# Performance work log

Hardware: AMD Instinct MI355X
Metric: run time of the kernel (lower is better)

## Reference

```python
import jax, jax.numpy as jnp
import numpy as np

BS, N, F_IN, H, F_OUT = 4, 2048, 128, 4, 64


def setup_inputs() -> dict:
    key = jax.random.key(0)
    k1, k2, k3, k4, k5 = jax.random.split(key, 5)
    x = jax.random.normal(k1, (BS, N, F_IN), dtype=jnp.float32)
    adj = jax.random.randint(k2, (BS, N, N), 0, 2).astype(bool)
    # guarantee self-loops so no softmax row is all -inf
    adj = jnp.logical_or(adj, jnp.eye(N, dtype=bool)[None])
    # xavier-uniform-ish scales
    w = jax.random.uniform(k3, (H, F_IN, F_OUT), dtype=jnp.float32,
                           minval=-1.0, maxval=1.0) * np.sqrt(6.0 / (F_IN + F_OUT))
    a_src = jax.random.uniform(k4, (H, F_OUT, 1), dtype=jnp.float32,
                               minval=-1.0, maxval=1.0) * np.sqrt(6.0 / (F_OUT + 1))
    a_dst = jax.random.uniform(k5, (H, F_OUT, 1), dtype=jnp.float32,
                               minval=-1.0, maxval=1.0) * np.sqrt(6.0 / (F_OUT + 1))
    bias = jnp.zeros((F_OUT,), dtype=jnp.float32)
    return {"x": x, "adj": adj, "w": w, "a_src": a_src, "a_dst": a_dst, "bias": bias}


def reference(x, adj, w, a_src, a_dst, bias):
    bs, n = x.shape[:2]
    # h_prime: [bs, H, n, F_OUT]
    h = jnp.einsum('bnf,hfo->bhno', x, w)
    th = jnp.tanh(h)
    s_src = jnp.einsum('bhno,ho->bhn', th, a_src[..., 0])  # [bs,H,n]
    s_dst = jnp.einsum('bhno,ho->bhn', th, a_dst[..., 0])  # [bs,H,n]
    # attn[b,h,i,j] = src[b,h,i] + dst[b,h,j]
    attn = s_src[..., :, None] + s_dst[..., None, :]
    attn = jnp.where(attn >= 0, attn, 0.2 * attn)  # leaky_relu(0.2)
    attn = jnp.where(adj[:, None], attn, -jnp.inf)  # mask = ~adj
    p = jax.nn.softmax(attn, axis=-1)  # dropout is identity at eval
    out = jnp.einsum('bhij,bhjo->bhio', p, h) + bias  # [bs,H,n,F_OUT]
    # torch .view(bs, n, -1) on contiguous [bs,H,n,F_OUT]: raw reshape
    return out.reshape(bs, n, -1)
```

## Files before the change

kernel.cpp:

```cpp
#include <hip/hip_runtime.h>
#include <hip/hip_fp16.h>

#define NN   2048
#define FIN  128
#define FOUT 64
#define LOG2E 1.44269504088896f

using f16x8 = __attribute__((ext_vector_type(8))) _Float16;
using f16x4 = __attribute__((ext_vector_type(4))) _Float16;
using f16x2 = __attribute__((ext_vector_type(2))) _Float16;
using f32x4 = __attribute__((ext_vector_type(4))) float;
using i32x4 = __attribute__((ext_vector_type(4))) int;

__device__ inline float fast_exp2(float x) {
#if __has_builtin(__builtin_amdgcn_exp2f)
    return __builtin_amdgcn_exp2f(x);
#else
    return exp2f(x);
#endif
}


__global__ __launch_bounds__(256) void k1_proj(
    const float* __restrict__ x, const float* __restrict__ w,
    const float* __restrict__ a_src, const float* __restrict__ a_dst,
    const int* __restrict__ adj,
    _Float16* __restrict__ h16B, float* __restrict__ ssrc, float* __restrict__ sdst,
    unsigned int* __restrict__ adjbits)
{
    __shared__ __align__(16) float w_s[FIN * FOUT];
    __shared__ __align__(16) float xs[64 * 132];

    const int t    = threadIdx.x;
    const int bx   = blockIdx.x;
    const int bh   = bx >> 5;
    const int tile = bx & 31;
    const int b    = bh >> 2;
    const int h    = bh & 3;
    const int n0   = tile * 64;

    {
        const f32x4* wg = (const f32x4*)(w + h * FIN * FOUT);
        f32x4* wl = (f32x4*)w_s;
#pragma unroll
        for (int k = 0; k < 8; ++k) wl[t + 256 * k] = wg[t + 256 * k];
    }
    {
#pragma unroll
        for (int k = 0; k < 8; ++k) {
            int q  = t + 256 * k;
            int r  = q >> 5;
            int c4 = q & 31;
            f32x4 v = *(const f32x4*)(x + (size_t)(b * NN + n0 + r) * FIN + c4 * 4);
            *(f32x4*)(xs + r * 132 + c4 * 4) = v;
        }
    }
    __syncthreads();

    const int ty = t >> 4, tx = t & 15;
    float acc[4][4] = {};

#pragma unroll 4
    for (int f4 = 0; f4 < 32; ++f4) {
        f32x4 xv[4], wv[4];
#pragma unroll
        for (int q = 0; q < 4; ++q)
            xv[q] = *(const f32x4*)(xs + (ty * 4 + q) * 132 + f4 * 4);
#pragma unroll
        for (int k = 0; k < 4; ++k)
            wv[k] = *(const f32x4*)(w_s + (f4 * 4 + k) * 64 + tx * 4);
#pragma unroll
        for (int q = 0; q < 4; ++q)
#pragma unroll
            for (int k = 0; k < 4; ++k)
#pragma unroll
                for (int c = 0; c < 4; ++c)
                    acc[q][c] += xv[q][k] * wv[k][c];
    }

    const int j0 = n0 + ty * 4;
#pragma unroll
    for (int cc = 0; cc < 4; ++cc) {
        int o = tx * 4 + cc;
        f16x4 hv;
#pragma unroll
        for (int q = 0; q < 4; ++q) hv[q] = (_Float16)acc[q][cc];
        int off = bh * 131072 + (j0 >> 5) * 2048 + (o >> 4) * 512
                + (((j0 >> 3) & 3) * 16 + (o & 15)) * 8 + (j0 & 7);
        *(f16x4*)(h16B + off) = hv;
    }

    f32x4 a_s = *(const f32x4*)(a_src + h * FOUT + tx * 4);
    f32x4 a_d = *(const f32x4*)(a_dst + h * FOUT + tx * 4);
    float ss[4], sd[4];
#pragma unroll
    for (int q = 0; q < 4; ++q) {
        float s1 = 0.f, s2 = 0.f;
#pragma unroll
        for (int cc = 0; cc < 4; ++cc) {
            float th = tanhf(acc[q][cc]);
            s1 += th * a_s[cc];
            s2 += th * a_d[cc];
        }
        ss[q] = s1; sd[q] = s2;
    }
#pragma unroll
    for (int m = 1; m <= 8; m <<= 1) {
#pragma unroll
        for (int q = 0; q < 4; ++q) {
            ss[q] += __shfl_xor(ss[q], m);
            sd[q] += __shfl_xor(sd[q], m);
        }
    }
    if (tx == 0) {
#pragma unroll
        for (int q = 0; q < 4; ++q) {
            ssrc[bh * NN + j0 + q] = ss[q] * LOG2E;
            sdst[bh * NN + j0 + q] = sd[q] * LOG2E;
        }
    }

    {
        const int  frow0 = bx * 16;
        const int* asrc  = adj + (size_t)frow0 * NN;
#pragma unroll
        for (int w4 = 0; w4 < 4; ++w4) {
            int widx  = t + 256 * w4;
            int row_l = widx >> 6;
            int wc    = widx & 63;
            const i32x4* p = (const i32x4*)(asrc + (size_t)row_l * NN + wc * 32);
            unsigned int wbits = 0;
#pragma unroll
            for (int k = 0; k < 8; ++k) {
                i32x4 v = p[k];
                wbits |= (unsigned int)(v[0] & 1) << (4 * k);
                wbits |= (unsigned int)(v[1] & 1) << (4 * k + 1);
                wbits |= (unsigned int)(v[2] & 1) << (4 * k + 2);
                wbits |= (unsigned int)(v[3] & 1) << (4 * k + 3);
            }
            adjbits[(size_t)(frow0 + row_l) * 64 + wc] = wbits;
        }
    }
}

__global__ __launch_bounds__(512, 6) void k2_attn(
    const unsigned int* __restrict__ adjbits,
    const _Float16* __restrict__ h16B,
    const float* __restrict__ ssrc, const float* __restrict__ sdst,
    const float* __restrict__ bias, float* __restrict__ out)
{
    __shared__ __align__(16) char smem[50240];
    _Float16*     Bf     = (_Float16*)smem;
    unsigned int* adjw   = (unsigned int*)(smem + 16384);
    float*        E1f    = (float*)(smem + 33792);
    float*        E2f    = (float*)(smem + 41984);
    float*        redmax = (float*)(smem + 50176);
    float*        comb   = (float*)smem;

    const int t    = threadIdx.x;
    const int wv   = t >> 6;
    const int lane = t & 63;
    const int bh   = blockIdx.x >> 5;
    const int i0   = (blockIdx.x & 31) << 6;
    const int b    = bh >> 2;
    const int rg   = wv >> 1;
    const int par  = wv & 1;
    const int m    = lane & 15;
    const int g    = lane >> 4;

    const _Float16* Bsrc = h16B + bh * 131072;

#define STAGE(bufi_, s_)                                                        \
    __builtin_amdgcn_global_load_lds(                                           \
        (const __attribute__((address_space(1))) unsigned int*)(Bsrc + (s_) * 4096 + t * 8), \
        (__attribute__((address_space(3))) unsigned int*)(Bf + (bufi_) * 4096 + t * 8), \
        16, 0, 0)

    STAGE(0, 0);

    {
        const uint4* asrc = (const uint4*)(adjbits + ((size_t)b * NN + i0) * 64);
#pragma unroll
        for (int k = 0; k < 2; ++k) {
            int idx = t + 512 * k;
            uint4 v = asrc[idx];
            unsigned int* dst = adjw + (idx >> 4) * 68 + (idx & 15) * 4;
            *(uint4*)dst = v;
        }
    }
    float dm;
    {
        f32x4 dv = *(const f32x4*)(sdst + bh * NN + t * 4);
        f32x4 e1v, e2v;
#pragma unroll
        for (int e = 0; e < 4; ++e) {
            e1v[e] = fast_exp2(dv[e]);
            e2v[e] = fast_exp2(0.2f * dv[e]);
        }
        *(f32x4*)(E1f + t * 4) = e1v;
        *(f32x4*)(E2f + t * 4) = e2v;
        dm = fmaxf(fmaxf(dv[0], dv[1]), fmaxf(dv[2], dv[3]));
#pragma unroll
        for (int msk = 1; msk <= 32; msk <<= 1) dm = fmaxf(dm, __shfl_xor(dm, msk));
        if (lane == 0) redmax[wv] = dm;
    }
    asm volatile("s_waitcnt vmcnt(0)" ::: "memory");
    __syncthreads();

    float D = redmax[0];
#pragma unroll
    for (int k = 1; k < 8; ++k) D = fmaxf(D, redmax[k]);

    const int row = i0 + rg * 16 + m;
    const float sA = ssrc[bh * NN + row];
    float c = sA + D; c = fmaxf(c, 0.2f * c);
    const float K1 = fast_exp2(sA - c);
    const float K2 = fast_exp2(fmaf(0.2f, sA, -c));

    f32x4 acc0 = {0,0,0,0}, acc1 = {0,0,0,0}, acc2 = {0,0,0,0}, acc3 = {0,0,0,0};
    f32x4 accz = {0,0,0,0};
    f16x8 ones;
#pragma unroll
    for (int i = 0; i < 8; ++i) ones[i] = (_Float16)1.0f;

    const int arow68 = (rg * 16 + m) * 68;

    for (int s = 0; s < 32; ++s) {
        if (s < 31) {
            STAGE((s + 1) & 1, s + 1);
            asm volatile("s_waitcnt vmcnt(1)" ::: "memory");
        } else {
            asm volatile("s_waitcnt vmcnt(0)" ::: "memory");
        }
        __builtin_amdgcn_sched_barrier(0);
        __builtin_amdgcn_s_barrier();
        __builtin_amdgcn_sched_barrier(0);

        const int ci = 2 * s + par;
        unsigned int wb = adjw[arow68 + ci] >> (8 * g);
        const float* e1p = E1f + ci * 32 + 8 * g;
        const float* e2p = E2f + ci * 32 + 8 * g;
        f32x4 e1a = *(const f32x4*)(e1p);
        f32x4 e1b = *(const f32x4*)(e1p + 4);
        f32x4 e2a = *(const f32x4*)(e2p);
        f32x4 e2b = *(const f32x4*)(e2p + 4);

        const _Float16* bb = Bf + (s & 1) * 4096 + par * 2048 + lane * 8;
        f16x8 b0 = *(const f16x8*)(bb);
        f16x8 b1 = *(const f16x8*)(bb + 512);
        f16x8 b2 = *(const f16x8*)(bb + 1024);
        f16x8 b3 = *(const f16x8*)(bb + 1536);

        float ev[8];
#pragma unroll
        for (int i = 0; i < 8; ++i) {
            float E1v = (i < 4) ? e1a[i] : e1b[i - 4];
            float E2v = (i < 4) ? e2a[i] : e2b[i - 4];
            float ee  = fmaxf(K1 * E1v, K2 * E2v);
            ev[i] = (wb & (1u << i)) ? ee : 0.0f;
        }
        union { f16x8 v; f16x2 p[4]; } af;
#pragma unroll
        for (int i = 0; i < 4; ++i)
            af.p[i] = __builtin_bit_cast(f16x2,
                __builtin_amdgcn_cvt_pkrtz(ev[2 * i], ev[2 * i + 1]));

        acc0 = __builtin_amdgcn_mfma_f32_16x16x32_f16(af.v, b0, acc0, 0, 0, 0);
        acc1 = __builtin_amdgcn_mfma_f32_16x16x32_f16(af.v, b1, acc1, 0, 0, 0);
        acc2 = __builtin_amdgcn_mfma_f32_16x16x32_f16(af.v, b2, acc2, 0, 0, 0);
        acc3 = __builtin_amdgcn_mfma_f32_16x16x32_f16(af.v, b3, acc3, 0, 0, 0);
        accz = __builtin_amdgcn_mfma_f32_16x16x32_f16(af.v, ones, accz, 0, 0, 0);

        __builtin_amdgcn_s_barrier();
    }
#undef STAGE

    __syncthreads();
    if (par == 1) {
        float* cp = comb + (rg * 64 + lane) * 20;
#pragma unroll
        for (int r = 0; r < 4; ++r) {
            cp[0 + r]  = acc0[r];
            cp[4 + r]  = acc1[r];
            cp[8 + r]  = acc2[r];
            cp[12 + r] = acc3[r];
            cp[16 + r] = accz[r];
        }
    }
    __syncthreads();
    if (par == 0) {
        const float* cp = comb + (rg * 64 + lane) * 20;
        float zs[4];
#pragma unroll
        for (int r = 0; r < 4; ++r) zs[r] = accz[r] + cp[16 + r];
        size_t obase = ((size_t)bh * NN + i0 + rg * 16) * FOUT;
#pragma unroll
        for (int ot = 0; ot < 4; ++ot) {
            float bv = bias[ot * 16 + m];
            f32x4 a = (ot == 0) ? acc0 : (ot == 1) ? acc1 : (ot == 2) ? acc2 : acc3;
#pragma unroll
            for (int r = 0; r < 4; ++r) {
                float v = (a[r] + cp[ot * 4 + r]) / zs[r] + bv;
                out[obase + (size_t)(g * 4 + r) * FOUT + ot * 16 + m] = v;
            }
        }
    }
}

extern "C" void kernel_launch(void* const* d_in, const int* in_sizes, int n_in,
                              void* d_out, int out_size, void* d_ws, size_t ws_size,
                              hipStream_t stream) {
    (void)in_sizes; (void)n_in; (void)out_size; (void)ws_size;
    const float* x     = (const float*)d_in[0];
    const int*   adj   = (const int*)d_in[1];
    const float* w     = (const float*)d_in[2];
    const float* a_src = (const float*)d_in[3];
    const float* a_dst = (const float*)d_in[4];
    const float* bias  = (const float*)d_in[5];
    float*       out   = (float*)d_out;

    _Float16*     h16B    = (_Float16*)d_ws;
    float*        ssrc    = (float*)((char*)d_ws + 4194304);
    float*        sdst    = (float*)((char*)d_ws + 4194304 + 131072);
    unsigned int* adjbits = (unsigned int*)((char*)d_ws + 4718592);

    k1_proj<<<512, 256, 0, stream>>>(x, w, a_src, a_dst, adj, h16B, ssrc, sdst, adjbits);
    k2_attn<<<512, 512, 0, stream>>>(adjbits, h16B, ssrc, sdst, bias, out);
}
```

Measured before the change: 50.58 us.

## Use MFMA fp16 projection, fast tanh, and packed fp16 attention weights

The projection kernel now converts x and w to fp16 in shared memory and computes the projection with MFMA instructions instead of scalar fp32 FMAs, and replaces tanhf with an exp2/rcp approximation. The attention kernel stores the exp tables in fp16, computes the attention weights with packed fp16 multiply/max plus a bitmask in place of per-element fp32 selects, and fully unrolls the main loop. This is meant to cut ALU and LDS work in both kernels. In exchange it loses precision in the projection, the scores, and the weight products (K times E is now computed in fp16, which could underflow or overflow), and the unroll grows code size.

```diff
diff --git a/kernel.cpp b/kernel.cpp
--- a/kernel.cpp
+++ b/kernel.cpp
@@ -18,6 +18,33 @@
 #else
     return exp2f(x);
 #endif
+}
+__device__ inline float fast_rcp(float x) {
+#if __has_builtin(__builtin_amdgcn_rcpf)
+    return __builtin_amdgcn_rcpf(x);
+#else
+    return 1.0f / x;
+#endif
+}
+__device__ inline float fast_tanh(float x) {
+    float e = fast_exp2(2.0f * LOG2E * x);
+    return 1.0f - 2.0f * fast_rcp(e + 1.0f);
+}
+__device__ inline unsigned cvt2h(float a, float b) {
+    return __builtin_bit_cast(unsigned, __builtin_amdgcn_cvt_pkrtz(a, b));
+}
+__device__ inline f16x2 pkmax(f16x2 a, f16x2 b) {
+#if __has_builtin(__builtin_elementwise_max)
+    return __builtin_elementwise_max(a, b);
+#else
+    f16x2 r; r[0] = a[0] > b[0] ? a[0] : b[0]; r[1] = a[1] > b[1] ? a[1] : b[1];
+    return r;
+#endif
+}
+__device__ inline unsigned bmask(unsigned wb, int p) {
+    unsigned lo = (unsigned)(-(int)((wb >> (2 * p)) & 1u));
+    unsigned hi = (unsigned)(-(int)((wb >> (2 * p + 1)) & 1u));
+    return (hi & 0xFFFF0000u) | (lo & 0x0000FFFFu);
 }
 
 
@@ -28,8 +55,8 @@
     _Float16* __restrict__ h16B, float* __restrict__ ssrc, float* __restrict__ sdst,
     unsigned int* __restrict__ adjbits)
 {
-    __shared__ __align__(16) float w_s[FIN * FOUT];
-    __shared__ __align__(16) float xs[64 * 132];
+    __shared__ __align__(16) _Float16 xf[8192];
+    __shared__ __align__(16) _Float16 wf[8192];
 
     const int t    = threadIdx.x;
     const int bx   = blockIdx.x;
@@ -38,85 +65,88 @@
     const int b    = bh >> 2;
     const int h    = bh & 3;
     const int n0   = tile * 64;
-
-    {
-        const f32x4* wg = (const f32x4*)(w + h * FIN * FOUT);
-        f32x4* wl = (f32x4*)w_s;
-#pragma unroll
-        for (int k = 0; k < 8; ++k) wl[t + 256 * k] = wg[t + 256 * k];
-    }
-    {
-#pragma unroll
-        for (int k = 0; k < 8; ++k) {
-            int q  = t + 256 * k;
-            int r  = q >> 5;
-            int c4 = q & 31;
-            f32x4 v = *(const f32x4*)(x + (size_t)(b * NN + n0 + r) * FIN + c4 * 4);
-            *(f32x4*)(xs + r * 132 + c4 * 4) = v;
+    const int wv   = t >> 6;
+    const int lane = t & 63;
+    const int m    = lane & 15;
+    const int g    = lane >> 4;
+
+    {
+        const int o  = t & 63;
+        const int kc = t >> 6;
+        const float* wcol = w + h * FIN * FOUT + o;
+        _Float16* dst = wf + ((kc * 4 + (o >> 4)) * 512) + (o & 15) * 8;
+#pragma unroll
+        for (int hi = 0; hi < 4; ++hi) {
+            unsigned u0 = cvt2h(wcol[(kc * 32 + hi * 8 + 0) * FOUT],
+                                wcol[(kc * 32 + hi * 8 + 1) * FOUT]);
+            unsigned u1 = cvt2h(wcol[(kc * 32 + hi * 8 + 2) * FOUT],
+                                wcol[(kc * 32 + hi * 8 + 3) * FOUT]);
+            unsigned u2 = cvt2h(wcol[(kc * 32 + hi * 8 + 4) * FOUT],
+                                wcol[(kc * 32 + hi * 8 + 5) * FOUT]);
+            unsigned u3 = cvt2h(wcol[(kc * 32 + hi * 8 + 6) * FOUT],
+                                wcol[(kc * 32 + hi * 8 + 7) * FOUT]);
+            *(uint4*)(dst + hi * 128) = uint4{u0, u1, u2, u3};
+        }
+    }
+    {
+        const int r  = t >> 2;
+        const int kc = t & 3;
+        const float* xr = x + ((size_t)(b * NN + n0 + r)) * FIN + kc * 32;
+        _Float16* dst = xf + ((r >> 4) * 16 + kc * 4) * 128 + (r & 15) * 8;
+#pragma unroll
+        for (int g2 = 0; g2 < 4; ++g2) {
+            f32x4 va = *(const f32x4*)(xr + g2 * 8);
+            f32x4 vb = *(const f32x4*)(xr + g2 * 8 + 4);
+            *(uint4*)(dst + g2 * 128) = uint4{cvt2h(va[0], va[1]), cvt2h(va[2], va[3]),
+                                              cvt2h(vb[0], vb[1]), cvt2h(vb[2], vb[3])};
         }
     }
     __syncthreads();
 
-    const int ty = t >> 4, tx = t & 15;
-    float acc[4][4] = {};
-
-#pragma unroll 4
-    for (int f4 = 0; f4 < 32; ++f4) {
-        f32x4 xv[4], wv[4];
-#pragma unroll
-        for (int q = 0; q < 4; ++q)
-            xv[q] = *(const f32x4*)(xs + (ty * 4 + q) * 132 + f4 * 4);
-#pragma unroll
-        for (int k = 0; k < 4; ++k)
-            wv[k] = *(const f32x4*)(w_s + (f4 * 4 + k) * 64 + tx * 4);
-#pragma unroll
-        for (int q = 0; q < 4; ++q)
-#pragma unroll
-            for (int k = 0; k < 4; ++k)
-#pragma unroll
-                for (int c = 0; c < 4; ++c)
-                    acc[q][c] += xv[q][k] * wv[k][c];
-    }
-
-    const int j0 = n0 + ty * 4;
-#pragma unroll
-    for (int cc = 0; cc < 4; ++cc) {
-        int o = tx * 4 + cc;
-        f16x4 hv;
-#pragma unroll
-        for (int q = 0; q < 4; ++q) hv[q] = (_Float16)acc[q][cc];
-        int off = bh * 131072 + (j0 >> 5) * 2048 + (o >> 4) * 512
-                + (((j0 >> 3) & 3) * 16 + (o & 15)) * 8 + (j0 & 7);
-        *(f16x4*)(h16B + off) = hv;
-    }
-
-    f32x4 a_s = *(const f32x4*)(a_src + h * FOUT + tx * 4);
-    f32x4 a_d = *(const f32x4*)(a_dst + h * FOUT + tx * 4);
-    float ss[4], sd[4];
-#pragma unroll
-    for (int q = 0; q < 4; ++q) {
-        float s1 = 0.f, s2 = 0.f;
-#pragma unroll
-        for (int cc = 0; cc < 4; ++cc) {
-            float th = tanhf(acc[q][cc]);
-            s1 += th * a_s[cc];
-            s2 += th * a_d[cc];
-        }
-        ss[q] = s1; sd[q] = s2;
-    }
-#pragma unroll
-    for (int m = 1; m <= 8; m <<= 1) {
-#pragma unroll
-        for (int q = 0; q < 4; ++q) {
-            ss[q] += __shfl_xor(ss[q], m);
-            sd[q] += __shfl_xor(sd[q], m);
-        }
-    }
-    if (tx == 0) {
-#pragma unroll
-        for (int q = 0; q < 4; ++q) {
-            ssrc[bh * NN + j0 + q] = ss[q] * LOG2E;
-            sdst[bh * NN + j0 + q] = sd[q] * LOG2E;
+    const int rg = wv;
+    f32x4 acc0 = {0,0,0,0}, acc1 = {0,0,0,0}, acc2 = {0,0,0,0}, acc3 = {0,0,0,0};
+#pragma unroll
+    for (int kc = 0; kc < 4; ++kc) {
+        f16x8 av = *(const f16x8*)(xf + (rg * 16 + kc * 4 + g) * 128 + m * 8);
+        const _Float16* wb_ = wf + kc * 4 * 512 + lane * 8;
+        acc0 = __builtin_amdgcn_mfma_f32_16x16x32_f16(av, *(const f16x8*)(wb_), acc0, 0, 0, 0);
+        acc1 = __builtin_amdgcn_mfma_f32_16x16x32_f16(av, *(const f16x8*)(wb_ + 512), acc1, 0, 0, 0);
+        acc2 = __builtin_amdgcn_mfma_f32_16x16x32_f16(av, *(const f16x8*)(wb_ + 1024), acc2, 0, 0, 0);
+        acc3 = __builtin_amdgcn_mfma_f32_16x16x32_f16(av, *(const f16x8*)(wb_ + 1536), acc3, 0, 0, 0);
+    }
+
+    float s1r[4] = {0,0,0,0}, s2r[4] = {0,0,0,0};
+    const int jg = n0 + rg * 16 + g * 4;
+#define PROC(accX, ot)  do {                                                    \
+        float asv = a_src[h * FOUT + (ot) * 16 + m];                            \
+        float adv = a_dst[h * FOUT + (ot) * 16 + m];                            \
+        _Pragma("unroll")                                                       \
+        for (int r = 0; r < 4; ++r) {                                           \
+            float th = fast_tanh(accX[r]);                                      \
+            s1r[r] += th * asv;                                                 \
+            s2r[r] += th * adv;                                                 \
+        }                                                                       \
+        unsigned u0 = cvt2h(accX[0], accX[1]);                                  \
+        unsigned u1 = cvt2h(accX[2], accX[3]);                                  \
+        int off = bh * 131072 + (jg >> 5) * 2048 + (ot) * 512                   \
+                + (((jg >> 3) & 3) * 16 + m) * 8 + (jg & 7);                    \
+        *(uint2*)(h16B + off) = uint2{u0, u1};                                  \
+    } while (0)
+    PROC(acc0, 0); PROC(acc1, 1); PROC(acc2, 2); PROC(acc3, 3);
+#undef PROC
+#pragma unroll
+    for (int msk = 1; msk <= 8; msk <<= 1) {
+#pragma unroll
+        for (int r = 0; r < 4; ++r) {
+            s1r[r] += __shfl_xor(s1r[r], msk);
+            s2r[r] += __shfl_xor(s2r[r], msk);
+        }
+    }
+    if (m == 0) {
+#pragma unroll
+        for (int r = 0; r < 4; ++r) {
+            ssrc[bh * NN + jg + r] = s1r[r] * LOG2E;
+            sdst[bh * NN + jg + r] = s2r[r] * LOG2E;
         }
     }
 
@@ -149,12 +179,12 @@
     const float* __restrict__ ssrc, const float* __restrict__ sdst,
     const float* __restrict__ bias, float* __restrict__ out)
 {
-    __shared__ __align__(16) char smem[50240];
+    __shared__ __align__(16) char smem[42016];
     _Float16*     Bf     = (_Float16*)smem;
     unsigned int* adjw   = (unsigned int*)(smem + 16384);
-    float*        E1f    = (float*)(smem + 33792);
-    float*        E2f    = (float*)(smem + 41984);
-    float*        redmax = (float*)(smem + 50176);
+    _Float16*     E1h    = (_Float16*)(smem + 33792);
+    _Float16*     E2h    = (_Float16*)(smem + 37888);
+    float*        redmax = (float*)(smem + 41984);
     float*        comb   = (float*)smem;
 
     const int t    = threadIdx.x;
@@ -177,28 +207,22 @@
         16, 0, 0)
 
     STAGE(0, 0);
-
     {
         const uint4* asrc = (const uint4*)(adjbits + ((size_t)b * NN + i0) * 64);
 #pragma unroll
         for (int k = 0; k < 2; ++k) {
             int idx = t + 512 * k;
             uint4 v = asrc[idx];
-            unsigned int* dst = adjw + (idx >> 4) * 68 + (idx & 15) * 4;
-            *(uint4*)dst = v;
+            *(uint4*)(adjw + (idx >> 4) * 68 + (idx & 15) * 4) = v;
         }
     }
     float dm;
     {
         f32x4 dv = *(const f32x4*)(sdst + bh * NN + t * 4);
-        f32x4 e1v, e2v;
-#pragma unroll
-        for (int e = 0; e < 4; ++e) {
-            e1v[e] = fast_exp2(dv[e]);
-            e2v[e] = fast_exp2(0.2f * dv[e]);
-        }
-        *(f32x4*)(E1f + t * 4) = e1v;
-        *(f32x4*)(E2f + t * 4) = e2v;
+        *(uint2*)(E1h + t * 4) = uint2{cvt2h(fast_exp2(dv[0]), fast_exp2(dv[1])),
+                                       cvt2h(fast_exp2(dv[2]), fast_exp2(dv[3]))};
+        *(uint2*)(E2h + t * 4) = uint2{cvt2h(fast_exp2(0.2f * dv[0]), fast_exp2(0.2f * dv[1])),
+                                       cvt2h(fast_exp2(0.2f * dv[2]), fast_exp2(0.2f * dv[3]))};
         dm = fmaxf(fmaxf(dv[0], dv[1]), fmaxf(dv[2], dv[3]));
 #pragma unroll
         for (int msk = 1; msk <= 32; msk <<= 1) dm = fmaxf(dm, __shfl_xor(dm, msk));
@@ -214,8 +238,10 @@
     const int row = i0 + rg * 16 + m;
     const float sA = ssrc[bh * NN + row];
     float c = sA + D; c = fmaxf(c, 0.2f * c);
-    const float K1 = fast_exp2(sA - c);
-    const float K2 = fast_exp2(fmaf(0.2f, sA, -c));
+    const float K1f = fast_exp2(sA - c);
+    const float K2f = fast_exp2(fmaf(0.2f, sA, -c));
+    f16x2 K1h2; { _Float16 q = (_Float16)K1f; K1h2[0] = q; K1h2[1] = q; }
+    f16x2 K2h2; { _Float16 q = (_Float16)K2f; K2h2[0] = q; K2h2[1] = q; }
 
     f32x4 acc0 = {0,0,0,0}, acc1 = {0,0,0,0}, acc2 = {0,0,0,0}, acc3 = {0,0,0,0};
     f32x4 accz = {0,0,0,0};
@@ -225,6 +251,7 @@
 
     const int arow68 = (rg * 16 + m) * 68;
 
+#pragma unroll
     for (int s = 0; s < 32; ++s) {
         if (s < 31) {
             STAGE((s + 1) & 1, s + 1);
@@ -237,13 +264,10 @@
         __builtin_amdgcn_sched_barrier(0);
 
         const int ci = 2 * s + par;
-        unsigned int wb = adjw[arow68 + ci] >> (8 * g);
-        const float* e1p = E1f + ci * 32 + 8 * g;
-        const float* e2p = E2f + ci * 32 + 8 * g;
-        f32x4 e1a = *(const f32x4*)(e1p);
-        f32x4 e1b = *(const f32x4*)(e1p + 4);
-        f32x4 e2a = *(const f32x4*)(e2p);
-        f32x4 e2b = *(const f32x4*)(e2p + 4);
+        unsigned wb = adjw[arow68 + ci] >> (8 * g);
+        union { f16x8 v; f16x2 p[4]; unsigned u[4]; } E1u, E2u, af;
+        E1u.v = *(const f16x8*)(E1h + ci * 32 + 8 * g);
+        E2u.v = *(const f16x8*)(E2h + ci * 32 + 8 * g);
 
         const _Float16* bb = Bf + (s & 1) * 4096 + par * 2048 + lane * 8;
         f16x8 b0 = *(const f16x8*)(bb);
@@ -251,19 +275,13 @@
         f16x8 b2 = *(const f16x8*)(bb + 1024);
         f16x8 b3 = *(const f16x8*)(bb + 1536);
 
-        float ev[8];
-#pragma unroll
-        for (int i = 0; i < 8; ++i) {
-            float E1v = (i < 4) ? e1a[i] : e1b[i - 4];
-            float E2v = (i < 4) ? e2a[i] : e2b[i - 4];
-            float ee  = fmaxf(K1 * E1v, K2 * E2v);
-            ev[i] = (wb & (1u << i)) ? ee : 0.0f;
-        }
-        union { f16x8 v; f16x2 p[4]; } af;
-#pragma unroll
-        for (int i = 0; i < 4; ++i)
-            af.p[i] = __builtin_bit_cast(f16x2,
-                __builtin_amdgcn_cvt_pkrtz(ev[2 * i], ev[2 * i + 1]));
+#pragma unroll
+        for (int p = 0; p < 4; ++p) {
+            f16x2 v1 = K1h2 * E1u.p[p];
+            f16x2 v2 = K2h2 * E2u.p[p];
+            f16x2 vm = pkmax(v1, v2);
+            af.u[p] = __builtin_bit_cast(unsigned, vm) & bmask(wb, p);
+        }
 
         acc0 = __builtin_amdgcn_mfma_f32_16x16x32_f16(af.v, b0, acc0, 0, 0, 0);
         acc1 = __builtin_amdgcn_mfma_f32_16x16x32_f16(af.v, b1, acc1, 0, 0, 0);
```

Result: faster. 41.31 us (-18.3%).
